# Optimization experiments

Measured on AMD Instinct MI355X. Metric: run time of the kernel, lower is better.

## Reference

```python
import jax, jax.numpy as jnp
import numpy as np

GROUPS = 8
EPS = 1e-5
V, CIN, COUT, K, TDIM, B = 49152, 128, 256, 8, 256, 1
E = V * 9


def group_norm(x, gamma, beta):
    # x: [B, V, C]; torch GroupNorm semantics: normalize over (pixels, channels-in-group)
    b, v, c = x.shape
    xg = x.reshape(b, v, GROUPS, c // GROUPS)
    mu = xg.mean(axis=(1, 3), keepdims=True)
    var = xg.var(axis=(1, 3), keepdims=True)
    xg = (xg - mu) * jax.lax.rsqrt(var + EPS)
    return xg.reshape(b, v, c) * gamma + beta


def cheb_conv(x, row, col, vals, w):
    # x: [B, V, C]; w: [K, C, F]; Chebyshev recurrence on sparse Laplacian
    b, v, c = x.shape
    k = w.shape[0]
    xt = x.transpose(1, 0, 2).reshape(v, b * c)  # [V, B*C]

    def spmv(z):  # sparse L @ z via scatter-add
        return jnp.zeros_like(z).at[row].add(vals[:, None] * z[col])

    terms = [xt]
    if k > 1:
        terms.append(spmv(xt))
    for _ in range(k - 2):
        terms.append(2.0 * spmv(terms[-1]) - terms[-2])
    t = jnp.stack(terms).reshape(k, v, b, c)  # [K, V, B, C]
    return jnp.einsum('kvbc,kcf->bvf', t, w)  # [B, V, F]


def setup_inputs() -> dict:
    key = jax.random.key(0)
    ks = jax.random.split(key, 12)
    return {
        'x': jax.random.normal(ks[0], (B, V, CIN), jnp.float32),
        'time_emb': jax.random.normal(ks[1], (B, TDIM), jnp.float32),
        'row': jax.random.randint(ks[2], (E,), 0, V),
        'col': jax.random.randint(ks[3], (E,), 0, V),
        'vals': jax.random.normal(ks[4], (E,), jnp.float32) * 0.1,
        'w_res': jax.random.normal(ks[5], (K, CIN, COUT), jnp.float32) * 0.05,
        'w1': jax.random.normal(ks[6], (K, CIN, COUT), jnp.float32) * 0.05,
        'w2': jax.random.normal(ks[7], (K, COUT, COUT), jnp.float32) * 0.05,
        'g1': jnp.ones((CIN,), jnp.float32),
        'b1': jnp.zeros((CIN,), jnp.float32),
        'g2': jnp.ones((COUT,), jnp.float32),
        'b2': jnp.zeros((COUT,), jnp.float32),
        'wt': jax.random.normal(ks[8], (TDIM, COUT), jnp.float32) * 0.05,
        'bt': jnp.zeros((COUT,), jnp.float32),
    }


def reference(x, time_emb, row, col, vals, w_res, w1, w2, g1, b1, g2, b2, wt, bt):
    # conv_res (in_channels != out_channels), pooling = identity
    res = cheb_conv(x, row, col, vals, w_res)
    # block1: conv(silu(group_norm(x)))
    h = cheb_conv(jax.nn.silu(group_norm(x, g1, b1)), row, col, vals, w1)
    # time embedding: SiLU -> Linear -> broadcast over pixels
    h = h + (jax.nn.silu(time_emb) @ wt + bt)[:, None, :]
    # block2
    h = cheb_conv(jax.nn.silu(group_norm(h, g2, b2)), row, col, vals, w2)
    return h + res
```

## Files before the change

### kernel.cpp

```cpp
#include <hip/hip_runtime.h>
#include <cstddef>

#define V_N 49152
#define E_N 442368
#define E_PAD 589824
#define GEPS 1e-5f
#define CO 256
#define TD 256

typedef _Float16 h16;
typedef _Float16 h8v __attribute__((ext_vector_type(8)));
typedef _Float16 h4v __attribute__((ext_vector_type(4)));
typedef float f4v __attribute__((ext_vector_type(4)));

__device__ __forceinline__ void gload_lds16(const void* g, void* l) {
    __builtin_amdgcn_global_load_lds(
        (const __attribute__((address_space(1))) unsigned int*)g,
        (__attribute__((address_space(3))) unsigned int*)l, 16, 0, 0);
}

__global__ void count_edges(const int* __restrict__ row, int* __restrict__ cnt) {
    int e = blockIdx.x * blockDim.x + threadIdx.x;
    if (e < E_N) atomicAdd(&cnt[row[e]], 1);
}

__global__ void scan_rowptr(int* __restrict__ cnt, int* __restrict__ rowptr) {
    __shared__ int part[1024];
    const int CHUNK = V_N / 1024;
    int t = threadIdx.x;
    int base = t * CHUNK;
    int s = 0;
    for (int i = 0; i < CHUNK; ++i) s += (cnt[base + i] + 3) & ~3;
    part[t] = s;
    __syncthreads();
    for (int off = 1; off < 1024; off <<= 1) {
        int v = part[t];
        int add = (t >= off) ? part[t - off] : 0;
        __syncthreads();
        part[t] = v + add;
        __syncthreads();
    }
    int run = (t == 0) ? 0 : part[t - 1];
    for (int i = 0; i < CHUNK; ++i) {
        int c = cnt[base + i];
        rowptr[base + i] = run;
        cnt[base + i] = run;
        run += (c + 3) & ~3;
    }
    if (t == 1023) rowptr[V_N] = run;
}

__global__ void fill_csr(const int* __restrict__ row, const int* __restrict__ col,
                         const float* __restrict__ vals, int* __restrict__ cursor,
                         int2* __restrict__ ep) {
    int e = blockIdx.x * blockDim.x + threadIdx.x;
    if (e < E_N) {
        int r = row[e];
        int slot = atomicAdd(&cursor[r], 1);
        ep[slot] = make_int2(col[e], __float_as_int(vals[e]));
    }
}

__global__ void wprep(const float* __restrict__ w, h16* __restrict__ wt, int KC) {
    __shared__ float t[16][17];
    int kc = blockIdx.x * 16 + threadIdx.y;
    int f = blockIdx.y * 16 + threadIdx.x;
    t[threadIdx.y][threadIdx.x] = w[(size_t)kc * CO + f];
    __syncthreads();
    int fo = blockIdx.y * 16 + threadIdx.y;
    int kco = blockIdx.x * 16 + threadIdx.x;
    wt[(size_t)fo * KC + kco] = (h16)t[threadIdx.x][threadIdx.y];
}

template <int C>
__global__ void gn_stats2(const float* __restrict__ x, const float* __restrict__ tvec,
                          float* __restrict__ part) {
    __shared__ float ls[8], lss[8];
    int t = threadIdx.x;
    if (t < 8) { ls[t] = 0.f; lss[t] = 0.f; }
    __syncthreads();
    const int total4 = V_N * (C / 4);
    const int cmask = (C / 4) - 1;
    const int stride = gridDim.x * blockDim.x;
    int i0 = blockIdx.x * blockDim.x + t;
    const int c4 = i0 & cmask;
    float t0 = 0.f, t1 = 0.f, t2 = 0.f, t3 = 0.f;
    if (tvec) {
        t0 = tvec[c4 * 4 + 0]; t1 = tvec[c4 * 4 + 1];
        t2 = tvec[c4 * 4 + 2]; t3 = tvec[c4 * 4 + 3];
    }
    float s = 0.f, ss = 0.f;
    for (int i = i0; i < total4; i += stride) {
        float4 v = ((const float4*)x)[i];
        v.x += t0; v.y += t1; v.z += t2; v.w += t3;
        s  += v.x + v.y + v.z + v.w;
        ss += v.x * v.x + v.y * v.y + v.z * v.z + v.w * v.w;
    }
    constexpr int GL = (C == 128) ? 4 : 8;
#pragma unroll
    for (int off = 1; off < GL; off <<= 1) {
        s  += __shfl_xor(s, off);
        ss += __shfl_xor(ss, off);
    }
    int lane = t & 63;
    if ((lane & (GL - 1)) == 0) {
        int g = c4 >> ((C == 128) ? 2 : 3);
        atomicAdd(&ls[g], s);
        atomicAdd(&lss[g], ss);
    }
    __syncthreads();
    if (t < 16) part[blockIdx.x * 16 + t] = (t < 8) ? ls[t] : lss[t - 8];
}

#define GN_BLOCKS 512

__global__ void gn_reduce(const float* __restrict__ part, float* __restrict__ stats,
                          int nb) {
    __shared__ float acc[16];
    int t = threadIdx.x;
    if (t < 16) acc[t] = 0.f;
    __syncthreads();
    int idx = t & 15;
    float s = 0.f;
    for (int j = t >> 4; j < nb; j += 16) s += part[j * 16 + idx];
    atomicAdd(&acc[idx], s);
    __syncthreads();
    if (t < 16) stats[t] = acc[t];
}

__global__ void gn1_apply(const float* __restrict__ x, const float* __restrict__ stats,
                          const float* __restrict__ gamma, const float* __restrict__ beta,
                          h16* __restrict__ dst, int ldT) {
    const float Ng = (float)V_N * 16.f;
    const int total4 = V_N * 32;
    for (int i = blockIdx.x * blockDim.x + threadIdx.x; i < total4;
         i += gridDim.x * blockDim.x) {
        int c4 = i & 31;
        int v = i >> 5;
        float4 xv = ((const float4*)x)[i];
        float in[4] = {xv.x, xv.y, xv.z, xv.w};
        h4v o, oc;
#pragma unroll
        for (int j = 0; j < 4; ++j) {
            int c = c4 * 4 + j;
            int g = c >> 4;
            float mu = stats[g] / Ng;
            float var = stats[8 + g] / Ng - mu * mu;
            float rs = rsqrtf(var + GEPS);
            float y = (in[j] - mu) * rs * gamma[c] + beta[c];
            y = y / (1.f + expf(-y));
            o[j] = (h16)y;
            oc[j] = (h16)in[j];
        }
        size_t base = (size_t)v * ldT + c4 * 4;
        *(h4v*)&dst[base] = o;
        *(h4v*)&dst[base + 128] = oc;
    }
}

__global__ void gn2_apply(const float* __restrict__ x, const float* __restrict__ tvec,
                          const float* __restrict__ stats, const float* __restrict__ gamma,
                          const float* __restrict__ beta, h16* __restrict__ dst, int ldT) {
    const float Ng = (float)V_N * 32.f;
    const int total4 = V_N * 64;
    for (int i = blockIdx.x * blockDim.x + threadIdx.x; i < total4;
         i += gridDim.x * blockDim.x) {
        int c4 = i & 63;
        int v = i >> 6;
        float4 xv = ((const float4*)x)[i];
        float in[4] = {xv.x, xv.y, xv.z, xv.w};
        h4v o;
#pragma unroll
        for (int j = 0; j < 4; ++j) {
            int c = c4 * 4 + j;
            int g = c >> 5;
            float mu = stats[g] / Ng;
            float var = stats[8 + g] / Ng - mu * mu;
            float rs = rsqrtf(var + GEPS);
            float val = in[j] + tvec[c];
            float y = (val - mu) * rs * gamma[c] + beta[c];
            y = y / (1.f + expf(-y));
            o[j] = (h16)y;
        }
        *(h4v*)&dst[(size_t)v * ldT + c4 * 4] = o;
    }
}

__global__ void time_mlp(const float* __restrict__ te, const float* __restrict__ wt,
                         const float* __restrict__ bt, float* __restrict__ tvec) {
    __shared__ float s[TD];
    int f = threadIdx.x;
    float v = te[f];
    s[f] = v / (1.f + expf(-v));
    __syncthreads();
    float acc = bt[f];
    for (int t = 0; t < TD; ++t) acc += s[t] * wt[t * CO + f];
    tvec[f] = acc;
}

template <bool RECUR>
__global__ void spmv2(const int* __restrict__ rowptr, const int2* __restrict__ ep,
                      const h16* __restrict__ zb, const h16* __restrict__ pb,
                      h16* __restrict__ db, int ldT) {
    int wid = threadIdx.x >> 6, lane = threadIdx.x & 63;
    int half = lane >> 5, hl = lane & 31;
    int v = blockIdx.x * 8 + wid * 2 + half;
    int s = rowptr[v], e = rowptr[v + 1];
    float acc[8];
#pragma unroll
    for (int i = 0; i < 8; ++i) acc[i] = 0.f;
    const int4* e4 = (const int4*)(ep + s);
    int n4 = (e - s) >> 1;
    for (int i = 0; i < n4; i += 2) {
        int4 a0 = e4[i], a1 = e4[i + 1];
        h8v z0 = *(const h8v*)&zb[(size_t)a0.x * ldT + hl * 8];
        h8v z1 = *(const h8v*)&zb[(size_t)a0.z * ldT + hl * 8];
        h8v z2 = *(const h8v*)&zb[(size_t)a1.x * ldT + hl * 8];
        h8v z3 = *(const h8v*)&zb[(size_t)a1.z * ldT + hl * 8];
        float v0 = __int_as_float(a0.y), v1 = __int_as_float(a0.w);
        float v2 = __int_as_float(a1.y), v3 = __int_as_float(a1.w);
#pragma unroll
        for (int k = 0; k < 8; ++k)
            acc[k] += v0 * (float)z0[k] + v1 * (float)z1[k] +
                      v2 * (float)z2[k] + v3 * (float)z3[k];
    }
    size_t base = (size_t)v * ldT + hl * 8;
    h8v o;
    if (RECUR) {
        h8v pv = *(const h8v*)&pb[base];
#pragma unroll
        for (int i = 0; i < 8; ++i) o[i] = (h16)(2.f * acc[i] - (float)pv[i]);
    } else {
#pragma unroll
        for (int i = 0; i < 8; ++i) o[i] = (h16)acc[i];
    }
    *(h8v*)&db[base] = o;
}

template <int MODE, bool DUAL>
__global__ __launch_bounds__(256, 6) void gemm_f16(
    const h16* __restrict__ A, int lda, const h16* __restrict__ Wt,
    const h16* __restrict__ Wt2, int ldw, int wofs, int KC, int ksh,
    const float* __restrict__ bias, float* __restrict__ out,
    float* __restrict__ out2) {
    __shared__ h16 As[2][64 * 32];
    __shared__ h16 Bs[2][128 * 32];
    if (DUAL && blockIdx.y) { A += 128; Wt = Wt2; out = out2; }
    const int bid = blockIdx.x;
    const int xcd = bid & 7;
    const int j = bid >> 3;
    const int mblk = xcd * 96 + (j >> 1);
    const int nh = j & 1;
    const int m0 = mblk * 64;
    const int n0 = nh * 128;
    const int tid = threadIdx.x;
    const int wid = tid >> 6, lane = tid & 63;
    const int fr = lane & 15, fq = lane >> 4;
    const int rl = lane >> 2;
    const int qs = (lane & 3) ^ ((lane >> 3) & 3);
    const int kmsk = (1 << ksh) - 1;
    const h16* Wb = Wt + wofs;
    const h16* Arow = A + (size_t)(m0 + wid * 16 + rl) * lda;
    const h16* Wrow = Wb + (size_t)(n0 + wid * 32 + rl) * ldw;

    f4v acc[4][2];
#pragma unroll
    for (int i = 0; i < 4; ++i)
#pragma unroll
        for (int n = 0; n < 2; ++n) acc[i][n] = (f4v){0.f, 0.f, 0.f, 0.f};

    const int nt = KC >> 5;
    {
        gload_lds16(Arow + qs * 8, &As[0][(wid * 16) * 32]);
#pragma unroll
        for (int j2 = 0; j2 < 2; ++j2)
            gload_lds16(Wrow + (size_t)(j2 * 16) * ldw + qs * 8,
                        &Bs[0][(wid * 32 + j2 * 16) * 32]);
    }
    __syncthreads();

    const int slot = (fq ^ ((fr >> 1) & 3)) * 8;
    for (int t = 0; t < nt; ++t) {
        const int cur = t & 1;
        h8v af[4], bf[2];
#pragma unroll
        for (int i = 0; i < 4; ++i)
            af[i] = *(const h8v*)&As[cur][(i * 16 + fr) * 32 + slot];
#pragma unroll
        for (int n = 0; n < 2; ++n)
            bf[n] = *(const h8v*)&Bs[cur][(wid * 32 + n * 16 + fr) * 32 + slot];
        if (t + 1 < nt) {
            int kk = (t + 1) << 5;
            int ca = (((kk >> ksh) << 8) | (kk & kmsk)) + qs * 8;
            int cb = kk + qs * 8;
            int nb = cur ^ 1;
            gload_lds16(Arow + ca, &As[nb][(wid * 16) * 32]);
#pragma unroll
            for (int j2 = 0; j2 < 2; ++j2)
                gload_lds16(Wrow + (size_t)(j2 * 16) * ldw + cb,
                            &Bs[nb][(wid * 32 + j2 * 16) * 32]);
        }
#pragma unroll
        for (int i = 0; i < 4; ++i)
#pragma unroll
            for (int n = 0; n < 2; ++n)
                acc[i][n] = __builtin_amdgcn_mfma_f32_16x16x32_f16(af[i], bf[n],
                                                                   acc[i][n], 0, 0, 0);
        __syncthreads();
    }
#pragma unroll
    for (int i = 0; i < 4; ++i)
#pragma unroll
        for (int n = 0; n < 2; ++n)
#pragma unroll
            for (int rr = 0; rr < 4; ++rr) {
                int row = m0 + i * 16 + fq * 4 + rr;
                int col = n0 + wid * 32 + n * 16 + fr;
                size_t idx = (size_t)row * CO + col;
                if (MODE == 0) out[idx] = acc[i][n][rr];
                else if (MODE == 1) out[idx] += acc[i][n][rr];
                else out[idx] = bias[idx] + acc[i][n][rr];
            }
}

static void chain_spmv(hipStream_t s, int chunk, int k0, int kend, h16* terms, int ldT,
                       const int* rp, const int2* ep) {
    for (int k = (k0 == 0 ? 1 : k0); k < kend; ++k) {
        const h16* zb = terms + ((k - 1) % chunk) * 256;
        h16* db = terms + (k % chunk) * 256;
        if (k == 1) {
            spmv2<false><<<V_N / 8, 256, 0, s>>>(rp, ep, zb, nullptr, db, ldT);
        } else {
            const h16* pb = terms + ((k - 2) % chunk) * 256;
            spmv2<true><<<V_N / 8, 256, 0, s>>>(rp, ep, zb, pb, db, ldT);
        }
    }
}

extern "C" void kernel_launch(void* const* d_in, const int* in_sizes, int n_in,
                              void* d_out, int out_size, void* d_ws, size_t ws_size,
                              hipStream_t stream) {
    const float* x    = (const float*)d_in[0];
    const float* te   = (const float*)d_in[1];
    const int*   row  = (const int*)d_in[2];
    const int*   col  = (const int*)d_in[3];
    const float* vals = (const float*)d_in[4];
    const float* wres = (const float*)d_in[5];
    const float* w1   = (const float*)d_in[6];
    const float* w2   = (const float*)d_in[7];
    const float* g1   = (const float*)d_in[8];
    const float* b1   = (const float*)d_in[9];
    const float* g2   = (const float*)d_in[10];
    const float* b2   = (const float*)d_in[11];
    const float* wt   = (const float*)d_in[12];
    const float* bt   = (const float*)d_in[13];
    float* out = (float*)d_out;

    const size_t slot_b = (size_t)V_N * 256 * 2;
    const size_t res_b  = (size_t)V_N * 256 * 4;
    const size_t csr_b  = (size_t)(V_N + V_N + 1) * 4 + (size_t)E_PAD * 8;
    const size_t wt_b   = (size_t)(1024 + 2048 + 1024) * CO * 2;
    const size_t misc_b = 8192 + (size_t)GN_BLOCKS * 16 * 4;
    auto need = [&](int ch) { return (size_t)ch * slot_b + res_b + csr_b + wt_b + misc_b; };
    int chunk = (ws_size >= need(8)) ? 8 : (ws_size >= need(4)) ? 4 : 2;
    if (ws_size < need(2)) return;
    const int ldT = chunk * 256;

    char* p = (char*)d_ws;
    h16* terms = (h16*)p;              p += (size_t)chunk * slot_b;
    float* resbuf = (float*)p;         p += res_b;
    h16* w1t = (h16*)p;                p += (size_t)1024 * CO * 2;
    h16* w2t = (h16*)p;                p += (size_t)2048 * CO * 2;
    h16* wrt = (h16*)p;                p += (size_t)1024 * CO * 2;
    int* cnt = (int*)p;                p += (size_t)V_N * 4;
    int* rp  = (int*)p;                p += (size_t)(V_N + 1) * 4;
    int2* ep = (int2*)p;               p += (size_t)E_PAD * 8;
    float* stats = (float*)p;          p += 64;
    float* tv = (float*)p;             p += 1024;
    float* gpart = (float*)p;          p += (size_t)GN_BLOCKS * 16 * 4;

    hipMemsetAsync(cnt, 0, V_N * sizeof(int), stream);
    hipMemsetAsync(ep, 0, (size_t)E_PAD * 8, stream);
    count_edges<<<E_N / 256, 256, 0, stream>>>(row, cnt);
    scan_rowptr<<<1, 1024, 0, stream>>>(cnt, rp);
    fill_csr<<<E_N / 256, 256, 0, stream>>>(row, col, vals, cnt, ep);

    wprep<<<dim3(1024 / 16, 16), dim3(16, 16), 0, stream>>>(w1, w1t, 1024);
    wprep<<<dim3(2048 / 16, 16), dim3(16, 16), 0, stream>>>(w2, w2t, 2048);
    wprep<<<dim3(1024 / 16, 16), dim3(16, 16), 0, stream>>>(wres, wrt, 1024);

    time_mlp<<<1, 256, 0, stream>>>(te, wt, bt, tv);

    gn_stats2<128><<<GN_BLOCKS, 256, 0, stream>>>(x, nullptr, gpart);
    gn_reduce<<<1, 256, 0, stream>>>(gpart, stats, GN_BLOCKS);
    gn1_apply<<<2048, 256, 0, stream>>>(x, stats, g1, b1, terms, ldT);

    for (int k0 = 0; k0 < 8; k0 += chunk) {
        int kend = (k0 + chunk < 8) ? k0 + chunk : 8;
        chain_spmv(stream, chunk, k0, kend, terms, ldT, rp, ep);
        int KC = (kend - k0) * 128;
        dim3 g(V_N / 64 * 2, 2);
        if (k0 == 0)
            gemm_f16<0, true><<<g, 256, 0, stream>>>(terms, ldT, w1t, wrt, 1024,
                                                     k0 * 128, KC, 7, nullptr, out, resbuf);
        else
            gemm_f16<1, true><<<g, 256, 0, stream>>>(terms, ldT, w1t, wrt, 1024,
                                                     k0 * 128, KC, 7, nullptr, out, resbuf);
    }

    gn_stats2<256><<<GN_BLOCKS, 256, 0, stream>>>(out, tv, gpart);
    gn_reduce<<<1, 256, 0, stream>>>(gpart, stats, GN_BLOCKS);
    gn2_apply<<<2048, 256, 0, stream>>>(out, tv, stats, g2, b2, terms, ldT);

    for (int k0 = 0; k0 < 8; k0 += chunk) {
        int kend = (k0 + chunk < 8) ? k0 + chunk : 8;
        chain_spmv(stream, chunk, k0, kend, terms, ldT, rp, ep);
        int KC = (kend - k0) * 256;
        dim3 g(V_N / 64 * 2);
        if (k0 == 0)
            gemm_f16<2, false><<<g, 256, 0, stream>>>(terms, ldT, w2t, nullptr, 2048,
                                                      0, KC, 8, resbuf, out, nullptr);
        else
            gemm_f16<1, false><<<g, 256, 0, stream>>>(terms, ldT, w2t, nullptr, 2048,
                                                      k0 * 256, KC, 8, nullptr, out, nullptr);
    }
}
```

Baseline: 874.6 us.

## Enlarge GEMM tile to 128x128 and load weights directly into registers

New measurement: 929.7 us. +6.3%, slower.

```diff
diff --git a/kernel.cpp b/kernel.cpp
--- a/kernel.cpp
+++ b/kernel.cpp
@@ -238,84 +238,83 @@
 }
 
 template <int MODE, bool DUAL>
-__global__ __launch_bounds__(256, 6) void gemm_f16(
+__global__ __launch_bounds__(256, 3) void gemm_f16(
     const h16* __restrict__ A, int lda, const h16* __restrict__ Wt,
     const h16* __restrict__ Wt2, int ldw, int wofs, int KC, int ksh,
     const float* __restrict__ bias, float* __restrict__ out,
     float* __restrict__ out2) {
-    __shared__ h16 As[2][64 * 32];
-    __shared__ h16 Bs[2][128 * 32];
+    __shared__ h16 As[2][128 * 32];
     if (DUAL && blockIdx.y) { A += 128; Wt = Wt2; out = out2; }
     const int bid = blockIdx.x;
     const int xcd = bid & 7;
     const int j = bid >> 3;
-    const int mblk = xcd * 96 + (j >> 1);
+    const int mblk = xcd * 48 + (j >> 1);
     const int nh = j & 1;
-    const int m0 = mblk * 64;
+    const int m0 = mblk * 128;
     const int n0 = nh * 128;
     const int tid = threadIdx.x;
     const int wid = tid >> 6, lane = tid & 63;
+    const int wm = wid & 1, wn = wid >> 1;
     const int fr = lane & 15, fq = lane >> 4;
     const int rl = lane >> 2;
     const int qs = (lane & 3) ^ ((lane >> 3) & 3);
     const int kmsk = (1 << ksh) - 1;
     const h16* Wb = Wt + wofs;
-    const h16* Arow = A + (size_t)(m0 + wid * 16 + rl) * lda;
-    const h16* Wrow = Wb + (size_t)(n0 + wid * 32 + rl) * ldw;
-
-    f4v acc[4][2];
+    const h16* Arow0 = A + (size_t)(m0 + wid * 16 + rl) * lda;
+    const h16* Arow1 = A + (size_t)(m0 + (wid + 4) * 16 + rl) * lda;
+    const h16* Wlane = Wb + (size_t)(n0 + wn * 64 + fr) * ldw + fq * 8;
+
+    f4v acc[4][4];
 #pragma unroll
     for (int i = 0; i < 4; ++i)
 #pragma unroll
-        for (int n = 0; n < 2; ++n) acc[i][n] = (f4v){0.f, 0.f, 0.f, 0.f};
+        for (int n = 0; n < 4; ++n) acc[i][n] = (f4v){0.f, 0.f, 0.f, 0.f};
 
     const int nt = KC >> 5;
-    {
-        gload_lds16(Arow + qs * 8, &As[0][(wid * 16) * 32]);
-#pragma unroll
-        for (int j2 = 0; j2 < 2; ++j2)
-            gload_lds16(Wrow + (size_t)(j2 * 16) * ldw + qs * 8,
-                        &Bs[0][(wid * 32 + j2 * 16) * 32]);
-    }
+    auto stageA = [&](int t, int buf) {
+        int kk = t << 5;
+        int ca = (((kk >> ksh) << 8) | (kk & kmsk)) + qs * 8;
+        gload_lds16(Arow0 + ca, &As[buf][(wid * 16) * 32]);
+        gload_lds16(Arow1 + ca, &As[buf][((wid + 4) * 16) * 32]);
+    };
+    h8v bfc[4], bfn[4];
+    stageA(0, 0);
+#pragma unroll
+    for (int n = 0; n < 4; ++n)
+        bfc[n] = *(const h8v*)&Wlane[(size_t)(n * 16) * ldw];
     __syncthreads();
 
     const int slot = (fq ^ ((fr >> 1) & 3)) * 8;
     for (int t = 0; t < nt; ++t) {
         const int cur = t & 1;
-        h8v af[4], bf[2];
+        h8v af[4];
 #pragma unroll
         for (int i = 0; i < 4; ++i)
-            af[i] = *(const h8v*)&As[cur][(i * 16 + fr) * 32 + slot];
-#pragma unroll
-        for (int n = 0; n < 2; ++n)
-            bf[n] = *(const h8v*)&Bs[cur][(wid * 32 + n * 16 + fr) * 32 + slot];
-        if (t + 1 < nt) {
-            int kk = (t + 1) << 5;
-            int ca = (((kk >> ksh) << 8) | (kk & kmsk)) + qs * 8;
-            int cb = kk + qs * 8;
-            int nb = cur ^ 1;
-            gload_lds16(Arow + ca, &As[nb][(wid * 16) * 32]);
-#pragma unroll
-            for (int j2 = 0; j2 < 2; ++j2)
-                gload_lds16(Wrow + (size_t)(j2 * 16) * ldw + cb,
-                            &Bs[nb][(wid * 32 + j2 * 16) * 32]);
-        }
+            af[i] = *(const h8v*)&As[cur][(wm * 64 + i * 16 + fr) * 32 + slot];
+        int tn = (t + 1 < nt) ? t + 1 : t;
+        stageA(tn, cur ^ 1);
+        int kkn = tn << 5;
+#pragma unroll
+        for (int n = 0; n < 4; ++n)
+            bfn[n] = *(const h8v*)&Wlane[(size_t)(n * 16) * ldw + kkn];
 #pragma unroll
         for (int i = 0; i < 4; ++i)
 #pragma unroll
-            for (int n = 0; n < 2; ++n)
-                acc[i][n] = __builtin_amdgcn_mfma_f32_16x16x32_f16(af[i], bf[n],
+            for (int n = 0; n < 4; ++n)
+                acc[i][n] = __builtin_amdgcn_mfma_f32_16x16x32_f16(af[i], bfc[n],
                                                                    acc[i][n], 0, 0, 0);
         __syncthreads();
+#pragma unroll
+        for (int n = 0; n < 4; ++n) bfc[n] = bfn[n];
     }
 #pragma unroll
     for (int i = 0; i < 4; ++i)
 #pragma unroll
-        for (int n = 0; n < 2; ++n)
+        for (int n = 0; n < 4; ++n)
 #pragma unroll
             for (int rr = 0; rr < 4; ++rr) {
-                int row = m0 + i * 16 + fq * 4 + rr;
-                int col = n0 + wid * 32 + n * 16 + fr;
+                int row = m0 + wm * 64 + i * 16 + fq * 4 + rr;
+                int col = n0 + wn * 64 + n * 16 + fr;
                 size_t idx = (size_t)row * CO + col;
                 if (MODE == 0) out[idx] = acc[i][n][rr];
                 else if (MODE == 1) out[idx] += acc[i][n][rr];
@@ -399,7 +398,7 @@
         int kend = (k0 + chunk < 8) ? k0 + chunk : 8;
         chain_spmv(stream, chunk, k0, kend, terms, ldT, rp, ep);
         int KC = (kend - k0) * 128;
-        dim3 g(V_N / 64 * 2, 2);
+        dim3 g(V_N / 128 * 2, 2);
         if (k0 == 0)
             gemm_f16<0, true><<<g, 256, 0, stream>>>(terms, ldT, w1t, wrt, 1024,
                                                      k0 * 128, KC, 7, nullptr, out, resbuf);
@@ -416,7 +415,7 @@
         int kend = (k0 + chunk < 8) ? k0 + chunk : 8;
         chain_spmv(stream, chunk, k0, kend, terms, ldT, rp, ep);
         int KC = (kend - k0) * 256;
-        dim3 g(V_N / 64 * 2);
+        dim3 g(V_N / 128 * 2);
         if (k0 == 0)
             gemm_f16<2, false><<<g, 256, 0, stream>>>(terms, ldT, w2t, nullptr, 2048,
                                                       0, KC, 8, resbuf, out, nullptr);
```
